# Kernel optimization log

Measured on AMD Instinct MI355X. Metric: run time of the kernel, lower is better.

## Reference

```python
import jax, jax.numpy as jnp
import numpy as np

B = 256      # batch_size (molecules)
S = 160      # max atoms per molecule (static; equals true max by construction)
D = 128      # embed_dim / atom feature dim
H = 8        # num_heads
K = 128      # key_dim per head (Keras MHA second positional arg)
F = 256      # dense_dim
EPS = 1e-3   # Keras LayerNormalization default epsilon


def _lengths():
    # deterministic molecule sizes in [96, 160], max exactly 160 (at i=37)
    return 96 + (np.arange(B) * 7) % 65


def setup_inputs() -> dict:
    key = jax.random.key(0)
    ks = jax.random.split(key, 8)
    lengths = _lengths()
    N = int(lengths.sum())  # 32706
    mol = jnp.asarray(np.repeat(np.arange(B), lengths), dtype=jnp.int32)
    sc = 1.0 / np.sqrt(D)
    return {
        'atom_features': jax.random.normal(ks[0], (N, D), jnp.float32),
        'molecule_indicator': mol,
        'wq': jax.random.normal(ks[1], (D, H, K), jnp.float32) * sc,
        'bq': jnp.zeros((H, K), jnp.float32),
        'wk': jax.random.normal(ks[2], (D, H, K), jnp.float32) * sc,
        'bk': jnp.zeros((H, K), jnp.float32),
        'wv': jax.random.normal(ks[3], (D, H, K), jnp.float32) * sc,
        'bv': jnp.zeros((H, K), jnp.float32),
        'wo': jax.random.normal(ks[4], (H, K, D), jnp.float32) * (1.0 / np.sqrt(H * K)),
        'bo': jnp.zeros((D,), jnp.float32),
        'w1': jax.random.normal(ks[5], (D, F), jnp.float32) * sc,
        'b1': jnp.zeros((F,), jnp.float32),
        'w2': jax.random.normal(ks[6], (F, D), jnp.float32) * (1.0 / np.sqrt(F)),
        'b2': jnp.zeros((D,), jnp.float32),
        'g1': jnp.ones((D,), jnp.float32),
        'be1': jnp.zeros((D,), jnp.float32),
        'g2': jnp.ones((D,), jnp.float32),
        'be2': jnp.zeros((D,), jnp.float32),
    }


def _ln(x, g, b):
    m = jnp.mean(x, axis=-1, keepdims=True)
    v = jnp.mean(jnp.square(x - m), axis=-1, keepdims=True)
    return (x - m) * jax.lax.rsqrt(v + EPS) * g + b


def reference(atom_features, molecule_indicator, wq, bq, wk, bk, wv, bv,
              wo, bo, w1, b1, w2, b2, g1, be1, g2, be2):
    N = atom_features.shape[0]
    # --- PartitionPadding: scatter ragged atoms into dense [B, S, D] ---
    counts = jax.ops.segment_sum(jnp.ones((N,), jnp.int32), molecule_indicator,
                                 num_segments=B)
    starts = jnp.cumsum(counts) - counts                      # [B]
    pos = jnp.arange(N, dtype=jnp.int32) - starts[molecule_indicator]
    x = jnp.zeros((B, S, D), atom_features.dtype).at[molecule_indicator, pos].set(atom_features)
    # (all molecules nonempty -> the original's all-zero-row gather is identity)
    mask = jnp.any(x != 0.0, axis=-1)                          # [B, S]
    num = jnp.sum(mask.astype(jnp.float32), axis=-1, keepdims=True)  # [B, 1]
    # --- Keras MultiHeadAttention (key mask only) ---
    q = jnp.einsum('bsd,dhk->bshk', x, wq) + bq
    k = jnp.einsum('bsd,dhk->bshk', x, wk) + bk
    v = jnp.einsum('bsd,dhk->bshk', x, wv) + bv
    scores = jnp.einsum('bqhk,bshk->bhqs', q, k) / jnp.sqrt(jnp.float32(K))
    scores = jnp.where(mask[:, None, None, :], scores, jnp.float32(-1e9))
    attn = jax.nn.softmax(scores, axis=-1)
    o = jnp.einsum('bhqs,bshk->bqhk', attn, v)
    attn_out = jnp.einsum('bqhk,hkd->bqd', o, wo) + bo
    # --- residual + LN + FFN + LN ---
    h = _ln(x + attn_out, g1, be1)
    ffn = jnp.maximum(h @ w1 + b1, 0.0) @ w2 + b2
    out = _ln(h + ffn, g2, be2)
    # --- masked mean readout (sums all rows, divides by true atom count) ---
    return jnp.sum(out, axis=1) / num
```

## Files before the change

### kernel.cpp

```cpp
#include <hip/hip_runtime.h>
#include <hip/hip_bf16.h>

typedef __attribute__((ext_vector_type(8))) short s16x8;
typedef __attribute__((ext_vector_type(4))) float f32x4;

__device__ __forceinline__ float bf_lo(unsigned u){ return __uint_as_float(u << 16); }
__device__ __forceinline__ float bf_hi(unsigned u){ return __uint_as_float(u & 0xFFFF0000u); }
__device__ __forceinline__ unsigned short f2bf(float f){
  unsigned u = __float_as_uint(f);
  u += 0x7FFFu + ((u >> 16) & 1u);
  return (unsigned short)(u >> 16);
}
__device__ __forceinline__ unsigned pk2(float lo, float hi){
  return (unsigned)f2bf(lo) | ((unsigned)f2bf(hi) << 16);
}
__device__ __forceinline__ float bf2f(unsigned short s){ return __uint_as_float(((unsigned)s) << 16); }
__device__ __forceinline__ s16x8 frg(uint4 u){ union { uint4 a; s16x8 b; } x; x.a = u; return x.b; }

#define VX(row) ((((row) & 3) << 4))

__device__ __forceinline__ float wredsum(float v){
  #pragma unroll
  for (int m = 32; m > 0; m >>= 1) v += __shfl_xor(v, m, 64);
  return v;
}
__device__ __forceinline__ float wredmax(float v){
  #pragma unroll
  for (int m = 32; m > 0; m >>= 1) v = fmaxf(v, __shfl_xor(v, m, 64));
  return v;
}

__global__ void k_prep_all(const float* __restrict__ wq, const float* __restrict__ wk,
                           const float* __restrict__ wv, const float* __restrict__ wo,
                           const float* __restrict__ w1, const float* __restrict__ w2,
                           const int* __restrict__ mol, int N,
                           unsigned short* __restrict__ wt,
                           unsigned short* __restrict__ w1t,
                           unsigned short* __restrict__ w2t,
                           int* __restrict__ starts){
  __shared__ float T[32][33];
  const int bid = blockIdx.x;
  const int t = threadIdx.x;
  if (bid < 512){
    const int mat = bid >> 7, h = (bid >> 4) & 7, tile = bid & 15;
    const int ti = tile >> 2, tj = tile & 3;
    const float* src; int rs;
    if (mat == 0){ src = wq + h * 128; rs = 1024; }
    else if (mat == 1){ src = wk + h * 128; rs = 1024; }
    else if (mat == 2){ src = wv + h * 128; rs = 1024; }
    else { src = wo + h * 16384; rs = 128; }
    for (int i = t; i < 1024; i += 256){
      const int r = i >> 5, cc = i & 31;
      T[r][cc] = src[(size_t)(tj * 32 + r) * rs + ti * 32 + cc];
    }
    __syncthreads();
    unsigned short* dst = wt + ((mat * 8 + h) << 14);
    for (int i = t; i < 1024; i += 256){
      const int orr = i >> 5, occ = i & 31;
      dst[(ti * 32 + orr) * 128 + tj * 32 + occ] = f2bf(T[occ][orr]);
    }
  } else if (bid < 544){
    const int bb = bid - 512;
    const int ti = bb >> 2, tj = bb & 3;
    for (int i = t; i < 1024; i += 256){
      const int r = i >> 5, cc = i & 31;
      T[r][cc] = w1[(size_t)(tj * 32 + r) * 256 + ti * 32 + cc];
    }
    __syncthreads();
    for (int i = t; i < 1024; i += 256){
      const int orr = i >> 5, occ = i & 31;
      w1t[(ti * 32 + orr) * 128 + tj * 32 + occ] = f2bf(T[occ][orr]);
    }
  } else if (bid < 576){
    const int bb = bid - 544;
    const int ti = bb >> 3, tj = bb & 7;
    for (int i = t; i < 1024; i += 256){
      const int r = i >> 5, cc = i & 31;
      T[r][cc] = w2[(size_t)(tj * 32 + r) * 128 + ti * 32 + cc];
    }
    __syncthreads();
    for (int i = t; i < 1024; i += 256){
      const int orr = i >> 5, occ = i & 31;
      w2t[(ti * 32 + orr) * 256 + tj * 32 + occ] = f2bf(T[occ][orr]);
    }
  } else {
    for (int i = t; i <= 256; i += 256){
      int lo = 0, hi = N;
      while (lo < hi){ const int m = (lo + hi) >> 1; if (mol[m] < i) lo = m + 1; else hi = m; }
      starts[i] = lo;
    }
  }
}

__global__ void k_starts(const int* __restrict__ mol, int N, int* __restrict__ starts){
  const int t = blockIdx.x * blockDim.x + threadIdx.x;
  if (t <= 256){
    int lo = 0, hi = N;
    while (lo < hi){ const int m = (lo + hi) >> 1; if (mol[m] < t) lo = m + 1; else hi = m; }
    starts[t] = lo;
  }
}

__global__ __launch_bounds__(512, 4) void k_attn3(
    const float* __restrict__ x, const unsigned short* __restrict__ wt,
    const float* __restrict__ bqg, const float* __restrict__ bkg, const float* __restrict__ bvg,
    const int* __restrict__ starts,
    unsigned short* __restrict__ aoh, unsigned short* __restrict__ qg, int N, int NR)
{
  __shared__ unsigned char SH[81920];
  const int bid = blockIdx.x;
  const int b = bid >> 3, h = bid & 7;
  const int st = starts[b];
  const int n  = starts[b + 1] - st;
  const int KTn = (n + 15) >> 4;
  const int QTn = (n + 16) >> 4;
  const int t = threadIdx.x, w = t >> 6, l = t & 63;
  const int c = l & 15, a = l >> 4;
  const f32x4 Z4 = {0.f, 0.f, 0.f, 0.f};
  unsigned char* Qg = (unsigned char*)qg + (size_t)bid * 45056;

  for (int i = t; i < 5120; i += 512){
    const int r = i >> 5, c4 = i & 31;
    uint2 v; v.x = 0u; v.y = 0u;
    if (r < n){
      const float4 xv = *(const float4*)(x + ((size_t)(st + r) << 7) + (c4 << 2));
      v.x = pk2(xv.x, xv.y); v.y = pk2(xv.z, xv.w);
    }
    *(uint2*)(&SH[r * 256 + ((c4 * 8) ^ ((r & 7) << 4))]) = v;
  }
  if (KTn & 1){
    const int dv = t >> 2, kq = t & 3;
    uint2 z; z.x = 0u; z.y = 0u;
    if (dv < 128) *(uint2*)(&SH[40960 + dv * 320 + ((KTn * 32 + kq * 8) ^ VX(dv))]) = z;
  }
  __syncthreads();

  const unsigned short* wqt = wt + ((0 * 8 + h) << 14);
  const unsigned short* wkt = wt + ((1 * 8 + h) << 14);
  const unsigned short* wvt = wt + ((2 * 8 + h) << 14);
  const unsigned short* wot = wt + ((3 * 8 + h) << 14);

  {
    f32x4 CQ[11];
    #pragma unroll
    for (int qt = 0; qt < 11; ++qt) CQ[qt] = Z4;
    #pragma unroll
    for (int kw = 0; kw < 4; ++kw){
      const s16x8 aq = frg(*(const uint4*)(wqt + (16 * w + c) * 128 + kw * 32 + a * 8));
      #pragma unroll
      for (int qt = 0; qt < 11; ++qt) if (qt < QTn){
        const int r0 = 16 * qt + c;
        const int row = r0 < 160 ? r0 : 159;
        const s16x8 xf = frg(*(const uint4*)(&SH[row * 256 + ((kw * 64 + a * 16) ^ ((row & 7) << 4))]));
        CQ[qt] = __builtin_amdgcn_mfma_f32_16x16x32_bf16(aq, xf, CQ[qt], 0, 0, 0);
      }
    }
    const float4 bq4 = *(const float4*)(bqg + h * 128 + 16 * w + 4 * a);
    const int kwq = w >> 1, ksq = 2 * (w & 1) + (a >> 1), half = a & 1;
    #pragma unroll
    for (int qt = 0; qt < 11; ++qt) if (qt < QTn){
      uint2 u;
      u.x = pk2(CQ[qt][0] + bq4.x, CQ[qt][1] + bq4.y);
      u.y = pk2(CQ[qt][2] + bq4.z, CQ[qt][3] + bq4.w);
      *(uint2*)(Qg + ((((qt * 4 + kwq) * 4 + ksq) * 16 + c) << 4) + 8 * half) = u;
    }
  }
  {
    f32x4 CK[10], CV[10];
    #pragma unroll
    for (int kt = 0; kt < 10; ++kt){ CK[kt] = Z4; CV[kt] = Z4; }
    #pragma unroll
    for (int kw = 0; kw < 4; ++kw){
      const int wofs = (16 * w + c) * 128 + kw * 32 + a * 8;
      const s16x8 ak  = frg(*(const uint4*)(wkt + wofs));
      const s16x8 bv8 = frg(*(const uint4*)(wvt + wofs));
      #pragma unroll
      for (int kt = 0; kt < 10; ++kt) if (kt < KTn){
        const int row = 16 * kt + c;
        const s16x8 xf = frg(*(const uint4*)(&SH[row * 256 + ((kw * 64 + a * 16) ^ ((row & 7) << 4))]));
        CK[kt] = __builtin_amdgcn_mfma_f32_16x16x32_bf16(ak, xf, CK[kt], 0, 0, 0);
        CV[kt] = __builtin_amdgcn_mfma_f32_16x16x32_bf16(xf, bv8, CV[kt], 0, 0, 0);
      }
    }
    const float bvv = bvg[h * 128 + 16 * w + c];
    #pragma unroll
    for (int kt = 0; kt < 10; ++kt) if (kt < KTn){
      uint2 v;
      v.x = pk2(CV[kt][0] + bvv, CV[kt][1] + bvv);
      v.y = pk2(CV[kt][2] + bvv, CV[kt][3] + bvv);
      *(uint2*)(&SH[40960 + (16 * w + c) * 320 + ((((16 * kt + 4 * a) << 1)) ^ VX(c))]) = v;
    }
    __syncthreads();
    const float4 bk4 = *(const float4*)(bkg + h * 128 + 16 * w + 4 * a);
    #pragma unroll
    for (int kt = 0; kt < 10; ++kt) if (kt < KTn){
      const int key = 16 * kt + c;
      uint2 u;
      u.x = pk2(CK[kt][0] + bk4.x, CK[kt][1] + bk4.y);
      u.y = pk2(CK[kt][2] + bk4.z, CK[kt][3] + bk4.w);
      *(uint2*)(&SH[key * 256 + ((32 * w + 8 * a) ^ ((key & 7) << 4))]) = u;
    }
  }
  __syncthreads();

  const float SCALE = 0.08838834764831845f;
  uint2 P[2][10];
  #pragma unroll
  for (int pass = 0; pass < 2; ++pass){
    const int qt = w + 8 * pass;
    if (qt < QTn){
      const int q = 16 * qt + c;
      f32x4 S[10];
      #pragma unroll
      for (int kt = 0; kt < 10; ++kt) S[kt] = Z4;
      #pragma unroll
      for (int kw = 0; kw < 4; ++kw){
        uint4 bu = *(const uint4*)(Qg + ((((qt * 4 + kw) * 4 + a) * 16 + c) << 4));
        if (q == 160){
          const float4 p0 = *(const float4*)(bqg + h * 128 + kw * 32 + 8 * a);
          const float4 p1 = *(const float4*)(bqg + h * 128 + kw * 32 + 8 * a + 4);
          bu.x = pk2(p0.x, p0.y); bu.y = pk2(p0.z, p0.w);
          bu.z = pk2(p1.x, p1.y); bu.w = pk2(p1.z, p1.w);
        }
        const s16x8 qb = frg(bu);
        #pragma unroll
        for (int kt = 0; kt < 10; ++kt) if (kt < KTn){
          const int krow = 16 * kt + c;
          const s16x8 kf = frg(*(const uint4*)(&SH[krow * 256 + ((kw * 64 + a * 16) ^ ((krow & 7) << 4))]));
          S[kt] = __builtin_amdgcn_mfma_f32_16x16x32_bf16(kf, qb, S[kt], 0, 0, 0);
        }
      }
      float mx = -3.0e38f;
      #pragma unroll
      for (int kt = 0; kt < 10; ++kt) if (kt < KTn){
        #pragma unroll
        for (int r = 0; r < 4; ++r){
          const int key = 16 * kt + 4 * a + r;
          const float sv = (key < n) ? S[kt][r] * SCALE : -1.0e30f;
          S[kt][r] = sv; mx = fmaxf(mx, sv);
        }
      }
      mx = fmaxf(mx, __shfl_xor(mx, 16, 64));
      mx = fmaxf(mx, __shfl_xor(mx, 32, 64));
      float sum = 0.f;
      #pragma unroll
      for (int kt = 0; kt < 10; ++kt) if (kt < KTn){
        #pragma unroll
        for (int r = 0; r < 4; ++r){
          const float e = __expf(S[kt][r] - mx);
          S[kt][r] = e; sum += e;
        }
      }
      sum += __shfl_xor(sum, 16, 64);
      sum += __shfl_xor(sum, 32, 64);
      const float inv = 1.f / sum;
      #pragma unroll
      for (int kt = 0; kt < 10; ++kt) if (kt < KTn){
        uint2 u;
        u.x = pk2(S[kt][0] * inv, S[kt][1] * inv);
        u.y = pk2(S[kt][2] * inv, S[kt][3] * inv);
        P[pass][kt] = u;
      }
    }
  }
  __syncthreads();

  const int pb = w * 5120;
  const int kwn = (KTn + 1) >> 1;
  #pragma unroll
  for (int pass = 0; pass < 2; ++pass){
    const int qt = w + 8 * pass;
    if (qt < QTn){
      const int q = 16 * qt + c;
      #pragma unroll
      for (int kt = 0; kt < 10; ++kt) if (kt < KTn)
        *(uint2*)(&SH[pb + c * 320 + ((((16 * kt + 4 * a) << 1)) ^ VX(c))]) = P[pass][kt];
      if (KTn & 1){
        uint2 z; z.x = 0u; z.y = 0u;
        *(uint2*)(&SH[pb + c * 320 + ((((16 * KTn + 4 * a) << 1)) ^ VX(c))]) = z;
      }
      f32x4 O[8];
      #pragma unroll
      for (int dt = 0; dt < 8; ++dt) O[dt] = Z4;
      for (int k2 = 0; k2 < kwn; ++k2){
        const s16x8 pf = frg(*(const uint4*)(&SH[pb + c * 320 + ((k2 * 64 + a * 16) ^ VX(c))]));
        #pragma unroll
        for (int dt = 0; dt < 8; ++dt){
          const s16x8 vf = frg(*(const uint4*)(&SH[40960 + (16 * dt + c) * 320 + ((k2 * 64 + a * 16) ^ VX(c))]));
          O[dt] = __builtin_amdgcn_mfma_f32_16x16x32_bf16(vf, pf, O[dt], 0, 0, 0);
        }
      }
      #pragma unroll
      for (int dt = 0; dt < 8; ++dt){
        uint2 u; u.x = pk2(O[dt][0], O[dt][1]); u.y = pk2(O[dt][2], O[dt][3]);
        *(uint2*)(&SH[pb + c * 320 + ((((16 * dt + 4 * a) << 1)) ^ VX(c))]) = u;
      }
      f32x4 AO[8];
      #pragma unroll
      for (int dt = 0; dt < 8; ++dt) AO[dt] = Z4;
      #pragma unroll
      for (int kw = 0; kw < 4; ++kw){
        const s16x8 ob = frg(*(const uint4*)(&SH[pb + c * 320 + ((kw * 64 + a * 16) ^ VX(c))]));
        #pragma unroll
        for (int dt = 0; dt < 8; ++dt){
          const s16x8 wf = frg(*(const uint4*)(wot + (16 * dt + c) * 128 + kw * 32 + a * 8));
          AO[dt] = __builtin_amdgcn_mfma_f32_16x16x32_bf16(wf, ob, AO[dt], 0, 0, 0);
        }
      }
      if (q <= n){
        const int grow = (q < n) ? (st + q) : (N + b);
        unsigned short* dst = aoh + (((size_t)h * NR + grow) << 7);
        #pragma unroll
        for (int dt = 0; dt < 8; ++dt){
          uint2 u; u.x = pk2(AO[dt][0], AO[dt][1]); u.y = pk2(AO[dt][2], AO[dt][3]);
          *(uint2*)(dst + 16 * dt + 4 * a) = u;
        }
      }
    }
  }
}

__global__ __launch_bounds__(512, 2) void k_attn(
    const float* __restrict__ x, const unsigned short* __restrict__ wt,
    const float* __restrict__ bqg, const float* __restrict__ bkg, const float* __restrict__ bvg,
    const int* __restrict__ starts,
    unsigned short* aoh, float* aof, int useslab, int N, int NR)
{
  __shared__ unsigned char SH[163840];
  const int b = blockIdx.x >> 3, h = blockIdx.x & 7;
  const int st = starts[b];
  const int n  = starts[b + 1] - st;
  const int KTn = (n + 15) >> 4;
  const int QTn = (n + 16) >> 4;
  const int t = threadIdx.x, w = t >> 6, l = t & 63;
  const int c = l & 15, a = l >> 4;
  const f32x4 Z4 = {0.f, 0.f, 0.f, 0.f};

  for (int i = t; i < 5120; i += 512){
    const int r = i >> 5, c4 = i & 31;
    uint2 v; v.x = 0u; v.y = 0u;
    if (r < n){
      const float4 xv = *(const float4*)(x + ((size_t)(st + r) << 7) + (c4 << 2));
      v.x = pk2(xv.x, xv.y); v.y = pk2(xv.z, xv.w);
    }
    *(uint2*)(&SH[r * 256 + ((c4 * 8) ^ ((r & 7) << 4))]) = v;
  }
  if (KTn & 1){
    const int dv = t >> 2, kq = t & 3;
    uint2 z; z.x = 0u; z.y = 0u;
    if (dv < 128) *(uint2*)(&SH[81920 + dv * 320 + ((KTn * 32 + kq * 8) ^ VX(dv))]) = z;
  }
  __syncthreads();

  const unsigned short* wqt = wt + ((0 * 8 + h) << 14);
  const unsigned short* wkt = wt + ((1 * 8 + h) << 14);
  const unsigned short* wvt = wt + ((2 * 8 + h) << 14);
  const unsigned short* wot = wt + ((3 * 8 + h) << 14);

  {
    f32x4 CK[10], CV[10];
    #pragma unroll
    for (int kt = 0; kt < 10; ++kt){ CK[kt] = Z4; CV[kt] = Z4; }
    #pragma unroll
    for (int kw = 0; kw < 4; ++kw){
      const int wofs = (16 * w + c) * 128 + kw * 32 + a * 8;
      const s16x8 ak  = frg(*(const uint4*)(wkt + wofs));
      const s16x8 bv8 = frg(*(const uint4*)(wvt + wofs));
      #pragma unroll
      for (int kt = 0; kt < 10; ++kt) if (kt < KTn){
        const int row = 16 * kt + c;
        const s16x8 xf = frg(*(const uint4*)(&SH[row * 256 + ((kw * 64 + a * 16) ^ ((row & 7) << 4))]));
        CK[kt] = __builtin_amdgcn_mfma_f32_16x16x32_bf16(ak, xf, CK[kt], 0, 0, 0);
        CV[kt] = __builtin_amdgcn_mfma_f32_16x16x32_bf16(xf, bv8, CV[kt], 0, 0, 0);
      }
    }
    const float4 bk4 = *(const float4*)(bkg + h * 128 + 16 * w + 4 * a);
    const float  bvv = bvg[h * 128 + 16 * w + c];
    #pragma unroll
    for (int kt = 0; kt < 10; ++kt) if (kt < KTn){
      const int key = 16 * kt + c;
      uint2 u;
      u.x = pk2(CK[kt][0] + bk4.x, CK[kt][1] + bk4.y);
      u.y = pk2(CK[kt][2] + bk4.z, CK[kt][3] + bk4.w);
      *(uint2*)(&SH[40960 + key * 256 + ((32 * w + 8 * a) ^ ((key & 7) << 4))]) = u;
      uint2 v;
      v.x = pk2(CV[kt][0] + bvv, CV[kt][1] + bvv);
      v.y = pk2(CV[kt][2] + bvv, CV[kt][3] + bvv);
      *(uint2*)(&SH[81920 + (16 * w + c) * 320 + ((((16 * kt + 4 * a) << 1)) ^ VX(c))]) = v;
    }
  }
  {
    f32x4 CQ[11];
    #pragma unroll
    for (int qt = 0; qt < 11; ++qt) CQ[qt] = Z4;
    #pragma unroll
    for (int kw = 0; kw < 4; ++kw){
      const s16x8 aq = frg(*(const uint4*)(wqt + (16 * w + c) * 128 + kw * 32 + a * 8));
      #pragma unroll
      for (int qt = 0; qt < 11; ++qt) if (qt < QTn){
        const int r0 = 16 * qt + c;
        const int row = r0 < 160 ? r0 : 159;
        const s16x8 xf = frg(*(const uint4*)(&SH[row * 256 + ((kw * 64 + a * 16) ^ ((row & 7) << 4))]));
        CQ[qt] = __builtin_amdgcn_mfma_f32_16x16x32_bf16(aq, xf, CQ[qt], 0, 0, 0);
      }
    }
    __syncthreads();
    const float4 bq4 = *(const float4*)(bqg + h * 128 + 16 * w + 4 * a);
    #pragma unroll
    for (int qt = 0; qt < 11; ++qt) if (qt < QTn){
      const int q = 16 * qt + c;
      if (q < 160){
        uint2 u;
        u.x = pk2(CQ[qt][0] + bq4.x, CQ[qt][1] + bq4.y);
        u.y = pk2(CQ[qt][2] + bq4.z, CQ[qt][3] + bq4.w);
        *(uint2*)(&SH[q * 256 + ((32 * w + 8 * a) ^ ((q & 7) << 4))]) = u;
      }
    }
  }
  __syncthreads();

  const float SCALE = 0.08838834764831845f;
  const int pb = 122880 + w * 5120;
  for (int qt = w; qt < QTn; qt += 8){
    const int q = 16 * qt + c;
    f32x4 S[10];
    #pragma unroll
    for (int kt = 0; kt < 10; ++kt) S[kt] = Z4;
    #pragma unroll
    for (int kw = 0; kw < 4; ++kw){
      const int qrow = q < 160 ? q : 159;
      uint4 bu = *(const uint4*)(&SH[qrow * 256 + ((kw * 64 + a * 16) ^ ((qrow & 7) << 4))]);
      if (q == 160){
        const float4 p0 = *(const float4*)(bqg + h * 128 + kw * 32 + a * 8);
        const float4 p1 = *(const float4*)(bqg + h * 128 + kw * 32 + a * 8 + 4);
        bu.x = pk2(p0.x, p0.y); bu.y = pk2(p0.z, p0.w);
        bu.z = pk2(p1.x, p1.y); bu.w = pk2(p1.z, p1.w);
      }
      const s16x8 qb = frg(bu);
      #pragma unroll
      for (int kt = 0; kt < 10; ++kt) if (kt < KTn){
        const int krow = 16 * kt + c;
        const s16x8 kf = frg(*(const uint4*)(&SH[40960 + krow * 256 + ((kw * 64 + a * 16) ^ ((krow & 7) << 4))]));
        S[kt] = __builtin_amdgcn_mfma_f32_16x16x32_bf16(kf, qb, S[kt], 0, 0, 0);
      }
    }
    float mx = -3.0e38f;
    #pragma unroll
    for (int kt = 0; kt < 10; ++kt) if (kt < KTn){
      #pragma unroll
      for (int r = 0; r < 4; ++r){
        const int key = 16 * kt + 4 * a + r;
        const float sv = (key < n) ? S[kt][r] * SCALE : -1.0e30f;
        S[kt][r] = sv; mx = fmaxf(mx, sv);
      }
    }
    mx = fmaxf(mx, __shfl_xor(mx, 16, 64));
    mx = fmaxf(mx, __shfl_xor(mx, 32, 64));
    float sum = 0.f;
    #pragma unroll
    for (int kt = 0; kt < 10; ++kt) if (kt < KTn){
      #pragma unroll
      for (int r = 0; r < 4; ++r){
        const float e = __expf(S[kt][r] - mx);
        S[kt][r] = e; sum += e;
      }
    }
    sum += __shfl_xor(sum, 16, 64);
    sum += __shfl_xor(sum, 32, 64);
    const float inv = 1.f / sum;
    #pragma unroll
    for (int kt = 0; kt < 10; ++kt) if (kt < KTn){
      uint2 u;
      u.x = pk2(S[kt][0] * inv, S[kt][1] * inv);
      u.y = pk2(S[kt][2] * inv, S[kt][3] * inv);
      *(uint2*)(&SH[pb + c * 320 + ((((16 * kt + 4 * a) << 1)) ^ VX(c))]) = u;
    }
    if (KTn & 1){
      uint2 z; z.x = 0u; z.y = 0u;
      *(uint2*)(&SH[pb + c * 320 + ((((16 * KTn + 4 * a) << 1)) ^ VX(c))]) = z;
    }
    f32x4 O[8];
    #pragma unroll
    for (int dt = 0; dt < 8; ++dt) O[dt] = Z4;
    const int kwn = (KTn + 1) >> 1;
    for (int k2 = 0; k2 < kwn; ++k2){
      const s16x8 pf = frg(*(const uint4*)(&SH[pb + c * 320 + ((k2 * 64 + a * 16) ^ VX(c))]));
      #pragma unroll
      for (int dt = 0; dt < 8; ++dt){
        const s16x8 vf = frg(*(const uint4*)(&SH[81920 + (16 * dt + c) * 320 + ((k2 * 64 + a * 16) ^ VX(c))]));
        O[dt] = __builtin_amdgcn_mfma_f32_16x16x32_bf16(vf, pf, O[dt], 0, 0, 0);
      }
    }
    #pragma unroll
    for (int dt = 0; dt < 8; ++dt){
      uint2 u; u.x = pk2(O[dt][0], O[dt][1]); u.y = pk2(O[dt][2], O[dt][3]);
      *(uint2*)(&SH[pb + c * 320 + ((((16 * dt + 4 * a) << 1)) ^ VX(c))]) = u;
    }
    f32x4 AO[8];
    #pragma unroll
    for (int dt = 0; dt < 8; ++dt) AO[dt] = Z4;
    #pragma unroll
    for (int kw = 0; kw < 4; ++kw){
      const s16x8 ob = frg(*(const uint4*)(&SH[pb + c * 320 + ((kw * 64 + a * 16) ^ VX(c))]));
      #pragma unroll
      for (int dt = 0; dt < 8; ++dt){
        const s16x8 wf = frg(*(const uint4*)(wot + (16 * dt + c) * 128 + kw * 32 + a * 8));
        AO[dt] = __builtin_amdgcn_mfma_f32_16x16x32_bf16(wf, ob, AO[dt], 0, 0, 0);
      }
    }
    if (q <= n){
      const int grow = (q < n) ? (st + q) : (N + b);
      if (useslab){
        unsigned short* dst = aoh + (((size_t)h * NR + grow) << 7);
        #pragma unroll
        for (int dt = 0; dt < 8; ++dt){
          uint2 u; u.x = pk2(AO[dt][0], AO[dt][1]); u.y = pk2(AO[dt][2], AO[dt][3]);
          *(uint2*)(dst + 16 * dt + 4 * a) = u;
        }
      } else {
        float* dstf = aof + ((size_t)grow << 7);
        #pragma unroll
        for (int dt = 0; dt < 8; ++dt){
          #pragma unroll
          for (int r = 0; r < 4; ++r)
            atomicAdd(dstf + 16 * dt + 4 * a + r, AO[dt][r]);
        }
      }
    }
  }
}

__global__ __launch_bounds__(512, 4) void k_ffn(
    const float* __restrict__ x, const int* __restrict__ mol,
    const unsigned short* aoh, const float* aof, int useslab,
    const float* __restrict__ bo,
    const unsigned short* __restrict__ w1t, const unsigned short* __restrict__ w2t,
    const float* __restrict__ b1, const float* __restrict__ b2,
    const float* __restrict__ g1, const float* __restrict__ be1,
    const float* __restrict__ g2, const float* __restrict__ be2,
    const int* __restrict__ starts, float* __restrict__ acc,
    int N, int NR)
{
  __shared__ unsigned char FS[49152];
  const int t = threadIdx.x, w = t >> 6, l = t & 63;
  const int c = l & 15, a = l >> 4;
  const int rbase = blockIdx.x * 64;
  const f32x4 Z4 = {0.f, 0.f, 0.f, 0.f};

  const float2 bo2  = *(const float2*)(bo  + 2 * l);
  const float2 g12  = *(const float2*)(g1  + 2 * l);
  const float2 be12 = *(const float2*)(be1 + 2 * l);

  float hreg[8][2];

  #pragma unroll 1
  for (int i = 0; i < 8; ++i){
    const int lr = w * 8 + i;
    const int row = rbase + lr;
    float v0 = 0.f, v1 = 0.f;
    if (row < NR){
      if (row < N){
        const float2 xv = *(const float2*)(x + ((size_t)row << 7) + 2 * l);
        v0 = xv.x; v1 = xv.y;
      }
      if (useslab){
        #pragma unroll
        for (int hh = 0; hh < 8; ++hh){
          const unsigned u = *(const unsigned*)(aoh + (((size_t)hh * NR + row) << 7) + 2 * l);
          v0 += bf_lo(u); v1 += bf_hi(u);
        }
      } else {
        const float2 av = *(const float2*)(aof + ((size_t)row << 7) + 2 * l);
        v0 += av.x; v1 += av.y;
      }
      v0 += bo2.x; v1 += bo2.y;
    }
    const float mean = wredsum(v0 + v1) * (1.f / 128.f);
    const float d0 = v0 - mean, d1 = v1 - mean;
    const float var = wredsum(d0 * d0 + d1 * d1) * (1.f / 128.f);
    const float iv = rsqrtf(var + 1e-3f);
    float h0 = d0 * iv * g12.x + be12.x;
    float h1v = d1 * iv * g12.y + be12.y;
    if (row >= NR){ h0 = 0.f; h1v = 0.f; }
    hreg[i][0] = h0; hreg[i][1] = h1v;
    *(unsigned*)(&FS[lr * 256 + ((4 * l) ^ ((lr & 7) << 4))]) = pk2(h0, h1v);
  }
  __syncthreads();

  const int m = w >> 1, nh = w & 1;
  {
    f32x4 acc1[8];
    #pragma unroll
    for (int nt = 0; nt < 8; ++nt) acc1[nt] = Z4;
    const int arow = 16 * m + c;
    #pragma unroll
    for (int kw = 0; kw < 4; ++kw){
      const s16x8 af = frg(*(const uint4*)(&FS[arow * 256 + ((kw * 64 + a * 16) ^ ((arow & 7) << 4))]));
      #pragma unroll
      for (int nt = 0; nt < 8; ++nt){
        const int j = 128 * nh + 16 * nt + c;
        const s16x8 bf = frg(*(const uint4*)(w1t + j * 128 + kw * 32 + a * 8));
        acc1[nt] = __builtin_amdgcn_mfma_f32_16x16x32_bf16(af, bf, acc1[nt], 0, 0, 0);
      }
    }
    #pragma unroll
    for (int nt = 0; nt < 8; ++nt){
      const int j = 128 * nh + 16 * nt + c;
      const float b1v = b1[j];
      #pragma unroll
      for (int rr = 0; rr < 4; ++rr){
        const int row = 16 * m + 4 * a + rr;
        const float vv = fmaxf(acc1[nt][rr] + b1v, 0.f);
        *(unsigned short*)(&FS[16384 + row * 512 + ((2 * j) ^ ((row & 7) << 4))]) = f2bf(vv);
      }
    }
  }
  __syncthreads();

  {
    f32x4 acc2[4];
    #pragma unroll
    for (int nt = 0; nt < 4; ++nt) acc2[nt] = Z4;
    const int arow = 16 * m + c;
    #pragma unroll
    for (int kw = 0; kw < 8; ++kw){
      const s16x8 af = frg(*(const uint4*)(&FS[16384 + arow * 512 + ((kw * 64 + a * 16) ^ ((arow & 7) << 4))]));
      #pragma unroll
      for (int nt = 0; nt < 4; ++nt){
        const int dd = 64 * nh + 16 * nt + c;
        const s16x8 bf = frg(*(const uint4*)(w2t + dd * 256 + kw * 32 + a * 8));
        acc2[nt] = __builtin_amdgcn_mfma_f32_16x16x32_bf16(af, bf, acc2[nt], 0, 0, 0);
      }
    }
    __syncthreads();
    #pragma unroll
    for (int nt = 0; nt < 4; ++nt){
      const int dd = 64 * nh + 16 * nt + c;
      #pragma unroll
      for (int rr = 0; rr < 4; ++rr){
        const int row = 16 * m + 4 * a + rr;
        *(float*)(&FS[16384 + row * 512 + ((4 * dd) ^ ((row & 4) << 4))]) = acc2[nt][rr];
      }
    }
  }
  __syncthreads();

  const float2 b22  = *(const float2*)(b2  + 2 * l);
  const float2 g22  = *(const float2*)(g2  + 2 * l);
  const float2 be22 = *(const float2*)(be2 + 2 * l);
  int curmb = -1; float s0 = 0.f, s1 = 0.f;
  #pragma unroll 1
  for (int i = 0; i < 8; ++i){
    const int lr = w * 8 + i;
    const int row = rbase + lr;
    if (row >= NR) continue;
    const float2 fv = *(const float2*)(&FS[16384 + lr * 512 + ((8 * l) ^ ((lr & 4) << 4))]);
    const float r0 = hreg[i][0] + fv.x + b22.x;
    const float r1 = hreg[i][1] + fv.y + b22.y;
    const float mean = wredsum(r0 + r1) * (1.f / 128.f);
    const float d0 = r0 - mean, d1 = r1 - mean;
    const float var = wredsum(d0 * d0 + d1 * d1) * (1.f / 128.f);
    const float iv = rsqrtf(var + 1e-3f);
    const float o0 = d0 * iv * g22.x + be22.x;
    const float o1 = d1 * iv * g22.y + be22.y;
    int mb; float wgt;
    if (row < N){ mb = mol[row]; wgt = 1.f; }
    else { mb = row - N; wgt = (float)(160 - (starts[mb + 1] - starts[mb])); }
    if (mb != curmb){
      if (curmb >= 0){
        atomicAdd(&acc[curmb * 128 + 2 * l],     s0);
        atomicAdd(&acc[curmb * 128 + 2 * l + 1], s1);
      }
      curmb = mb; s0 = o0 * wgt; s1 = o1 * wgt;
    } else {
      s0 += o0 * wgt; s1 += o1 * wgt;
    }
  }
  if (curmb >= 0){
    atomicAdd(&acc[curmb * 128 + 2 * l],     s0);
    atomicAdd(&acc[curmb * 128 + 2 * l + 1], s1);
  }
}

#define LDK 130
__global__ __launch_bounds__(512, 2) void k_attn_v(
    const float* __restrict__ x,
    const float* __restrict__ wq, const float* __restrict__ bq,
    const float* __restrict__ wk, const float* __restrict__ bk,
    const float* __restrict__ wv, const float* __restrict__ bv,
    const float* __restrict__ wo,
    const int* __restrict__ starts, float* __restrict__ ao, int N)
{
  __shared__ unsigned short Qs[161 * LDK];
  __shared__ unsigned short Ks[160 * LDK];
  __shared__ unsigned short Vs[160 * LDK];

  const int b = blockIdx.x >> 3, h = blockIdx.x & 7;
  const int st = starts[b];
  const int n  = starts[b + 1] - st;
  const int nq = n + 1;
  const float* X = x + (size_t)st * 128;
  const int t = threadIdx.x;
  const int k = t & 127, sg = t >> 7;
  const int w = t >> 6,  l = t & 63;

  {
    const float bqv = bq[h * 128 + k], bkv = bk[h * 128 + k], bvv = bv[h * 128 + k];
    const float* wqc = wq + h * 128 + k;
    const float* wkc = wk + h * 128 + k;
    const float* wvc = wv + h * 128 + k;
    const int per = (nq + 3) >> 2;
    const int r0  = sg * per;
    for (int cch = 0; cch < 3; ++cch){
      const int rb = r0 + cch * 16;
      if (rb >= nq) break;
      const float4* xrp[16];
      #pragma unroll
      for (int i = 0; i < 16; ++i){
        int rr = rb + i; int rc = rr < n ? rr : (n - 1);
        xrp[i] = (const float4*)X + (size_t)rc * 32;
      }
      float aq[16], ak[16], av[16];
      #pragma unroll
      for (int i = 0; i < 16; ++i){ aq[i] = bqv; ak[i] = bkv; av[i] = bvv; }
      #pragma unroll 1
      for (int dq = 0; dq < 32; ++dq){
        float4 xv[16];
        #pragma unroll
        for (int i = 0; i < 16; ++i) xv[i] = xrp[i][dq];
        #pragma unroll
        for (int e = 0; e < 4; ++e){
          const int d = dq * 4 + e;
          const float wqv = wqc[d * 1024];
          const float wkv = wkc[d * 1024];
          const float wvv = wvc[d * 1024];
          #pragma unroll
          for (int i = 0; i < 16; ++i){
            const float xs = (e == 0) ? xv[i].x : (e == 1) ? xv[i].y : (e == 2) ? xv[i].z : xv[i].w;
            aq[i] = fmaf(xs, wqv, aq[i]);
            ak[i] = fmaf(xs, wkv, ak[i]);
            av[i] = fmaf(xs, wvv, av[i]);
          }
        }
      }
      #pragma unroll
      for (int i = 0; i < 16; ++i){
        const int rr = rb + i;
        if (rr < n){
          Qs[rr * LDK + k] = f2bf(aq[i]);
          Ks[rr * LDK + k] = f2bf(ak[i]);
          Vs[rr * LDK + k] = f2bf(av[i]);
        } else if (rr == n){
          Qs[rr * LDK + k] = f2bf(bqv);
        }
      }
    }
  }
  __syncthreads();

  const float SCALE = 0.0883883476483184f;
  const int itn = (nq + 7) >> 3;
  for (int it = 0; it < itn; ++it){
    const int sq = w + it * 8;
    if (sq < nq){
      const unsigned* qrow = (const unsigned*)(Qs + sq * LDK);
      const int j0 = l, j1 = l + 64, j2 = l + 128;
      const unsigned* k0r = (const unsigned*)(Ks + j0 * LDK);
      const unsigned* k1r = (const unsigned*)(Ks + j1 * LDK);
      const unsigned* k2r = (const unsigned*)(Ks + (j2 < 160 ? j2 : 159) * LDK);
      float a0 = 0.f, a1 = 0.f, a2 = 0.f;
      #pragma unroll 8
      for (int kk = 0; kk < 64; ++kk){
        const unsigned uq = qrow[kk];
        const float ql = bf_lo(uq), qh = bf_hi(uq);
        const unsigned u0 = k0r[kk], u1 = k1r[kk], u2 = k2r[kk];
        a0 += ql * bf_lo(u0) + qh * bf_hi(u0);
        a1 += ql * bf_lo(u1) + qh * bf_hi(u1);
        a2 += ql * bf_lo(u2) + qh * bf_hi(u2);
      }
      const float s0 = (j0 < n) ? a0 * SCALE : -1e30f;
      const float s1 = (j1 < n) ? a1 * SCALE : -1e30f;
      const float s2 = (j2 < n) ? a2 * SCALE : -1e30f;
      const float m  = wredmax(fmaxf(s0, fmaxf(s1, s2)));
      const float e0 = __expf(s0 - m), e1 = __expf(s1 - m), e2 = __expf(s2 - m);
      const float inv = 1.f / wredsum(e0 + e1 + e2);
      const float p0 = e0 * inv, p1 = e1 * inv, p2 = e2 * inv;
      float o0 = 0.f, o1 = 0.f;
      const unsigned short* vp = Vs + 2 * l;
      #pragma unroll 4
      for (int j = 0; j < 64; ++j){
        const float pj = __shfl(p0, j, 64);
        const unsigned uv = *(const unsigned*)(vp + j * LDK);
        o0 = fmaf(pj, bf_lo(uv), o0);
        o1 = fmaf(pj, bf_hi(uv), o1);
      }
      const int n1 = n < 128 ? n : 128;
      #pragma unroll 4
      for (int j = 64; j < n1; ++j){
        const float pj = __shfl(p1, j - 64, 64);
        const unsigned uv = *(const unsigned*)(vp + j * LDK);
        o0 = fmaf(pj, bf_lo(uv), o0);
        o1 = fmaf(pj, bf_hi(uv), o1);
      }
      #pragma unroll 4
      for (int j = 128; j < n; ++j){
        const float pj = __shfl(p2, j - 128, 64);
        const unsigned uv = *(const unsigned*)(vp + j * LDK);
        o0 = fmaf(pj, bf_lo(uv), o0);
        o1 = fmaf(pj, bf_hi(uv), o1);
      }
      ((unsigned*)(Qs + sq * LDK))[l] = pk2(o0, o1);
    }
  }
  __syncthreads();

  {
    const int d = k;
    const int per = (nq + 3) >> 2;
    const int r0  = sg * per;
    const int rend = min(r0 + per, nq);
    const float* wop = wo + (size_t)(h * 128) * 128 + d;
    for (int cch = 0; cch < 3; ++cch){
      const int rb = r0 + cch * 16;
      if (rb >= rend) break;
      int roff[16];
      #pragma unroll
      for (int i = 0; i < 16; ++i){
        int rr = rb + i;
        roff[i] = (rr < nq ? rr : (nq - 1)) * LDK;
      }
      float acc[16];
      #pragma unroll
      for (int i = 0; i < 16; ++i) acc[i] = 0.f;
      #pragma unroll 1
      for (int kk = 0; kk < 128; ++kk){
        const float wv2 = wop[(size_t)kk * 128];
        #pragma unroll
        for (int i = 0; i < 16; ++i)
          acc[i] = fmaf(bf2f(Qs[roff[i] + kk]), wv2, acc[i]);
      }
      #pragma unroll
      for (int i = 0; i < 16; ++i){
        const int rr = rb + i;
        if (rr < rend){
          const int grow = (rr < n) ? (st + rr) : (N + b);
          atomicAdd(&ao[(size_t)grow * 128 + d], acc[i]);
        }
      }
    }
  }
}

__global__ __launch_bounds__(512, 2) void k_ffn_v(
    const float* __restrict__ x, const int* __restrict__ mol,
    const float* __restrict__ ao, const float* __restrict__ bo,
    const float* __restrict__ w1, const float* __restrict__ b1,
    const float* __restrict__ w2, const float* __restrict__ b2,
    const float* __restrict__ g1, const float* __restrict__ be1,
    const float* __restrict__ g2, const float* __restrict__ be2,
    const int* __restrict__ starts, float* __restrict__ acc,
    int N, int NR)
{
  __shared__ unsigned short Ws[32768];
  __shared__ float h1s[32][128];
  __shared__ unsigned short ts[32][256];
  const int t = threadIdx.x, w = t >> 6, l = t & 63;
  const int rbase = blockIdx.x * 32;

  for (int i = t; i < 32768; i += 512) Ws[i] = f2bf(w1[i]);
  __syncthreads();

  for (int it = 0; it < 4; ++it){
    const int r = w + it * 8;
    const int row = rbase + r;
    if (row < NR){
      float x0 = 0.f, x1 = 0.f;
      if (row < N){
        x0 = x[(size_t)row * 128 + l];
        x1 = x[(size_t)row * 128 + l + 64];
      }
      const float a0 = x0 + ao[(size_t)row * 128 + l]      + bo[l];
      const float a1 = x1 + ao[(size_t)row * 128 + l + 64] + bo[l + 64];
      const float mean = wredsum(a0 + a1) * (1.f / 128.f);
      const float d0 = a0 - mean, d1 = a1 - mean;
      const float var = wredsum(d0 * d0 + d1 * d1) * (1.f / 128.f);
      const float inv = rsqrtf(var + 1e-3f);
      h1s[r][l]      = d0 * inv * g1[l]      + be1[l];
      h1s[r][l + 64] = d1 * inv * g1[l + 64] + be1[l + 64];
    }
    __syncthreads();
    if (row < NR){
      float tj0 = b1[l], tj1 = b1[l + 64], tj2 = b1[l + 128], tj3 = b1[l + 192];
      #pragma unroll 4
      for (int d = 0; d < 128; ++d){
        const float hv = h1s[r][d];
        tj0 = fmaf(hv, bf2f(Ws[d * 256 + l]),       tj0);
        tj1 = fmaf(hv, bf2f(Ws[d * 256 + l + 64]),  tj1);
        tj2 = fmaf(hv, bf2f(Ws[d * 256 + l + 128]), tj2);
        tj3 = fmaf(hv, bf2f(Ws[d * 256 + l + 192]), tj3);
      }
      ts[r][l]       = f2bf(fmaxf(tj0, 0.f));
      ts[r][l + 64]  = f2bf(fmaxf(tj1, 0.f));
      ts[r][l + 128] = f2bf(fmaxf(tj2, 0.f));
      ts[r][l + 192] = f2bf(fmaxf(tj3, 0.f));
    }
  }
  __syncthreads();
  for (int i = t; i < 32768; i += 512) Ws[i] = f2bf(w2[i]);
  __syncthreads();

  for (int it = 0; it < 4; ++it){
    const int r = w + it * 8;
    const int row = rbase + r;
    if (row >= NR) continue;
    float f0 = b2[l], f1 = b2[l + 64];
    #pragma unroll 4
    for (int j = 0; j < 256; ++j){
      const float tv = bf2f(ts[r][j]);
      f0 = fmaf(tv, bf2f(Ws[j * 128 + l]),      f0);
      f1 = fmaf(tv, bf2f(Ws[j * 128 + l + 64]), f1);
    }
    const float r0 = h1s[r][l] + f0, r1 = h1s[r][l + 64] + f1;
    const float mean = wredsum(r0 + r1) * (1.f / 128.f);
    const float d0 = r0 - mean, d1 = r1 - mean;
    const float var = wredsum(d0 * d0 + d1 * d1) * (1.f / 128.f);
    const float inv = rsqrtf(var + 1e-3f);
    const float o0 = d0 * inv * g2[l]      + be2[l];
    const float o1 = d1 * inv * g2[l + 64] + be2[l + 64];
    int mb; float wgt;
    if (row < N){ mb = mol[row]; wgt = 1.f; }
    else { mb = row - N; wgt = (float)(160 - (starts[mb + 1] - starts[mb])); }
    atomicAdd(&acc[mb * 128 + l],      o0 * wgt);
    atomicAdd(&acc[mb * 128 + l + 64], o1 * wgt);
  }
}

__global__ void k_out(const float* __restrict__ acc, const int* __restrict__ starts,
                      float* __restrict__ out){
  const int i = blockIdx.x * blockDim.x + threadIdx.x;
  if (i < 256 * 128){
    const int b = i >> 7;
    out[i] = acc[i] / (float)(starts[b + 1] - starts[b]);
  }
}

extern "C" void kernel_launch(void* const* d_in, const int* in_sizes, int n_in,
                              void* d_out, int out_size, void* d_ws, size_t ws_size,
                              hipStream_t stream)
{
  const float* x   = (const float*)d_in[0];
  const int*   mol = (const int*)d_in[1];
  const float* wq  = (const float*)d_in[2];
  const float* bq  = (const float*)d_in[3];
  const float* wk  = (const float*)d_in[4];
  const float* bk  = (const float*)d_in[5];
  const float* wv  = (const float*)d_in[6];
  const float* bv  = (const float*)d_in[7];
  const float* wo  = (const float*)d_in[8];
  const float* bo  = (const float*)d_in[9];
  const float* w1  = (const float*)d_in[10];
  const float* b1  = (const float*)d_in[11];
  const float* w2  = (const float*)d_in[12];
  const float* b2  = (const float*)d_in[13];
  const float* g1  = (const float*)d_in[14];
  const float* be1 = (const float*)d_in[15];
  const float* g2  = (const float*)d_in[16];
  const float* be2 = (const float*)d_in[17];

  const int N  = in_sizes[1];
  const int NR = N + 256;

  const size_t off_wt  = 2048;
  const size_t off_w1t = off_wt  + 1048576;
  const size_t off_w2t = off_w1t + 65536;
  const size_t off_acc = off_w2t + 65536;
  const size_t off_ao  = off_acc + 131072;
  const size_t off_q   = off_ao + (size_t)8 * NR * 128 * 2;
  const size_t need3 = off_q + (size_t)2048 * 45056;
  const size_t need2 = off_q;
  const size_t need1 = off_ao + (size_t)NR * 128 * 4;
  const int mode = (ws_size >= need3) ? 3 : (ws_size >= need2) ? 2
                 : (ws_size >= need1) ? 1 : 0;

  char* wsp = (char*)d_ws;
  int* starts = (int*)wsp;

  if (mode >= 1){
    unsigned short* wt  = (unsigned short*)(wsp + off_wt);
    unsigned short* w1t = (unsigned short*)(wsp + off_w1t);
    unsigned short* w2t = (unsigned short*)(wsp + off_w2t);
    float*          acc = (float*)(wsp + off_acc);
    unsigned short* aoh = (unsigned short*)(wsp + off_ao);
    float*          aof = (float*)(wsp + off_ao);
    unsigned short* qg  = (unsigned short*)(wsp + off_q);
    const int useslab = (mode >= 2) ? 1 : 0;

    hipMemsetAsync(acc, 0, 131072, stream);
    if (!useslab) hipMemsetAsync(aof, 0, (size_t)NR * 128 * 4, stream);
    k_prep_all<<<577, 256, 0, stream>>>(wq, wk, wv, wo, w1, w2, mol, N,
                                        wt, w1t, w2t, starts);
    if (mode == 3)
      k_attn3<<<2048, 512, 0, stream>>>(x, wt, bq, bk, bv, starts, aoh, qg, N, NR);
    else
      k_attn<<<2048, 512, 0, stream>>>(x, wt, bq, bk, bv, starts, aoh, aof, useslab, N, NR);
    k_ffn<<<(NR + 63) / 64, 512, 0, stream>>>(x, mol, aoh, aof, useslab, bo, w1t, w2t,
                                              b1, b2, g1, be1, g2, be2, starts, acc, N, NR);
    k_out<<<(256 * 128 + 255) / 256, 256, 0, stream>>>(acc, starts, (float*)d_out);
  } else {
    float* ao  = (float*)(wsp + 2048);
    float* acc = (float*)(wsp + 2048 + (size_t)NR * 128 * 4);
    hipMemsetAsync(ao, 0, (size_t)(NR + 256) * 128 * 4, stream);
    k_starts<<<1, 512, 0, stream>>>(mol, N, starts);
    k_attn_v<<<256 * 8, 512, 0, stream>>>(x, wq, bq, wk, bk, wv, bv, wo, starts, ao, N);
    k_ffn_v<<<(NR + 31) / 32, 512, 0, stream>>>(x, mol, ao, bo, w1, b1, w2, b2,
                                                g1, be1, g2, be2, starts, acc, N, NR);
    k_out<<<(256 * 128 + 255) / 256, 256, 0, stream>>>(acc, starts, (float*)d_out);
  }
}
```

Measured before the change: 263.6 us.

## Fold output projection into V before attention-weighted sum

Precomputes VW = V·Wo per head for the keys (one MFMA pass over key tiles) and stores it transposed in LDS, so the per-query-tile P·V product directly yields the projected output. This removes the intermediate O round-trip through LDS and the separate O·Wo MFMA loop per query tile. The cost is an extra GEMM over keys (KTn tiles instead of QTn tiles), scalar 16-bit LDS stores for V, an extra bf16 rounding of V before the product and an extra barrier.

```diff
diff --git a/kernel.cpp b/kernel.cpp
--- a/kernel.cpp
+++ b/kernel.cpp
@@ -128,11 +128,6 @@
     }
     *(uint2*)(&SH[r * 256 + ((c4 * 8) ^ ((r & 7) << 4))]) = v;
   }
-  if (KTn & 1){
-    const int dv = t >> 2, kq = t & 3;
-    uint2 z; z.x = 0u; z.y = 0u;
-    if (dv < 128) *(uint2*)(&SH[40960 + dv * 320 + ((KTn * 32 + kq * 8) ^ VX(dv))]) = z;
-  }
   __syncthreads();
 
   const unsigned short* wqt = wt + ((0 * 8 + h) << 14);
@@ -185,10 +180,12 @@
     const float bvv = bvg[h * 128 + 16 * w + c];
     #pragma unroll
     for (int kt = 0; kt < 10; ++kt) if (kt < KTn){
-      uint2 v;
-      v.x = pk2(CV[kt][0] + bvv, CV[kt][1] + bvv);
-      v.y = pk2(CV[kt][2] + bvv, CV[kt][3] + bvv);
-      *(uint2*)(&SH[40960 + (16 * w + c) * 320 + ((((16 * kt + 4 * a) << 1)) ^ VX(c))]) = v;
+      #pragma unroll
+      for (int r = 0; r < 4; ++r){
+        const int key = 16 * kt + 4 * a + r;
+        *(unsigned short*)(&SH[40960 + key * 256 +
+            ((((16 * w + c) << 1)) ^ ((key & 7) << 4))]) = f2bf(CV[kt][r] + bvv);
+      }
     }
     __syncthreads();
     const float4 bk4 = *(const float4*)(bkg + h * 128 + 16 * w + 4 * a);
@@ -263,6 +260,33 @@
       }
     }
   }
+
+  f32x4 CW[10];
+  #pragma unroll
+  for (int kt = 0; kt < 10; ++kt) CW[kt] = Z4;
+  #pragma unroll
+  for (int kw = 0; kw < 4; ++kw){
+    const s16x8 wf = frg(*(const uint4*)(wot + (16 * w + c) * 128 + kw * 32 + a * 8));
+    #pragma unroll
+    for (int kt = 0; kt < 10; ++kt) if (kt < KTn){
+      const int row = 16 * kt + c;
+      const s16x8 vf = frg(*(const uint4*)(&SH[40960 + row * 256 + ((kw * 64 + a * 16) ^ ((row & 7) << 4))]));
+      CW[kt] = __builtin_amdgcn_mfma_f32_16x16x32_bf16(vf, wf, CW[kt], 0, 0, 0);
+    }
+  }
+  __syncthreads();
+
+  #pragma unroll
+  for (int kt = 0; kt < 10; ++kt) if (kt < KTn){
+    uint2 u;
+    u.x = pk2(CW[kt][0], CW[kt][1]);
+    u.y = pk2(CW[kt][2], CW[kt][3]);
+    *(uint2*)(&SH[40960 + (16 * w + c) * 320 + ((((16 * kt + 4 * a) << 1)) ^ VX(c))]) = u;
+  }
+  if (KTn & 1){
+    uint2 z; z.x = 0u; z.y = 0u;
+    *(uint2*)(&SH[40960 + (16 * w + c) * 320 + ((((16 * KTn + 4 * a) << 1)) ^ VX(c))]) = z;
+  }
   __syncthreads();
 
   const int pb = w * 5120;
@@ -279,32 +303,15 @@
         uint2 z; z.x = 0u; z.y = 0u;
         *(uint2*)(&SH[pb + c * 320 + ((((16 * KTn + 4 * a) << 1)) ^ VX(c))]) = z;
       }
-      f32x4 O[8];
-      #pragma unroll
-      for (int dt = 0; dt < 8; ++dt) O[dt] = Z4;
+      f32x4 AO[8];
+      #pragma unroll
+      for (int dt = 0; dt < 8; ++dt) AO[dt] = Z4;
       for (int k2 = 0; k2 < kwn; ++k2){
         const s16x8 pf = frg(*(const uint4*)(&SH[pb + c * 320 + ((k2 * 64 + a * 16) ^ VX(c))]));
         #pragma unroll
         for (int dt = 0; dt < 8; ++dt){
-          const s16x8 vf = frg(*(const uint4*)(&SH[40960 + (16 * dt + c) * 320 + ((k2 * 64 + a * 16) ^ VX(c))]));
-          O[dt] = __builtin_amdgcn_mfma_f32_16x16x32_bf16(vf, pf, O[dt], 0, 0, 0);
-        }
-      }
-      #pragma unroll
-      for (int dt = 0; dt < 8; ++dt){
-        uint2 u; u.x = pk2(O[dt][0], O[dt][1]); u.y = pk2(O[dt][2], O[dt][3]);
-        *(uint2*)(&SH[pb + c * 320 + ((((16 * dt + 4 * a) << 1)) ^ VX(c))]) = u;
-      }
-      f32x4 AO[8];
-      #pragma unroll
-      for (int dt = 0; dt < 8; ++dt) AO[dt] = Z4;
-      #pragma unroll
-      for (int kw = 0; kw < 4; ++kw){
-        const s16x8 ob = frg(*(const uint4*)(&SH[pb + c * 320 + ((kw * 64 + a * 16) ^ VX(c))]));
-        #pragma unroll
-        for (int dt = 0; dt < 8; ++dt){
-          const s16x8 wf = frg(*(const uint4*)(wot + (16 * dt + c) * 128 + kw * 32 + a * 8));
-          AO[dt] = __builtin_amdgcn_mfma_f32_16x16x32_bf16(wf, ob, AO[dt], 0, 0, 0);
+          const s16x8 vwf = frg(*(const uint4*)(&SH[40960 + (16 * dt + c) * 320 + ((k2 * 64 + a * 16) ^ VX(c))]));
+          AO[dt] = __builtin_amdgcn_mfma_f32_16x16x32_bf16(vwf, pf, AO[dt], 0, 0, 0);
         }
       }
       if (q <= n){
```

Result: faster. 224.9 us (-14.7%).
